# Performance work log

Measured on AMD Instinct MI355X. Metric: run time of the kernel, lower is better.

## Reference

```python
import jax, jax.numpy as jnp
import numpy as np

N, T, E, F, H, L, NC = 50000, 5, 500000, 64, 4, 2, 8192
NEG_SLOPE = 0.2  # PyG GATConv LeakyReLU slope


def _gat(x, src, dst, W, a_s, a_d, b):
    # x: [N,Fin], W: [Fin,H*F] -> h: [N,H,F]
    h = (x @ W).reshape(N, H, F)
    al = (h * a_s).sum(-1)                      # [N,H] alpha_src per node
    ar = (h * a_d).sum(-1)                      # [N,H] alpha_dst per node
    e = jax.nn.leaky_relu(al[src] + ar[dst], NEG_SLOPE)   # [Etot,H]
    m = jax.ops.segment_max(e, dst, num_segments=N)       # stable softmax per dst
    ex = jnp.exp(e - m[dst])
    den = jax.ops.segment_sum(ex, dst, num_segments=N)
    alpha = ex / (den[dst] + 1e-16)
    out = jax.ops.segment_sum(h[src] * alpha[:, :, None], dst, num_segments=N)
    return out.reshape(N, H * F) + b


def _gnn_stack(x, src, dst, gW, gas, gad, gb, lW, lb):
    for i in range(L):
        x = _gat(x, src, dst, gW[i], gas[i], gad[i], gb[i])
        x = jax.nn.relu(x @ lW[i] + lb[i])
    return x


def _snapshots(embeddings, edges, gW, gas, gad, gb, lW, lb):
    loop = jnp.arange(N)
    outs = []
    for t in range(T):
        src = jnp.concatenate([edges[t, 0], loop])  # add self loops (PyG default)
        dst = jnp.concatenate([edges[t, 1], loop])
        outs.append(_gnn_stack(embeddings[t], src, dst, gW, gas, gad, gb, lW, lb))
    # torch code prepends each snapshot -> time axis is reversed
    return jnp.stack(outs[::-1], axis=1)  # [N, T, F]


def _lstm(xs, Wi, Wh, b):
    # xs: [T,B,D]; torch gate order i,f,g,o
    B = xs.shape[1]
    hid = Wh.shape[1]
    def step(carry, x):
        h, c = carry
        g = x @ Wi.T + h @ Wh.T + b
        i, f, gg, o = jnp.split(g, 4, axis=-1)
        c = jax.nn.sigmoid(f) * c + jax.nn.sigmoid(i) * jnp.tanh(gg)
        h = jax.nn.sigmoid(o) * jnp.tanh(c)
        return (h, c), h
    init = (jnp.zeros((B, hid), xs.dtype), jnp.zeros((B, hid), xs.dtype))
    (hT, _), hs = jax.lax.scan(step, init, xs)
    return hs, hT


def setup_inputs() -> dict:
    key = jax.random.key(0)
    ks = iter(jax.random.split(key, 40))
    def nrm(shape, scale=0.1):
        return jax.random.normal(next(ks), shape, dtype=jnp.float32) * scale
    inp = {
        "embeddings": jax.random.normal(next(ks), (T, N, F), dtype=jnp.float32),
        "gat1_W": nrm((L, F, H * F)), "gat1_as": nrm((L, H, F)), "gat1_ad": nrm((L, H, F)), "gat1_b": nrm((L, H * F)),
        "lin1_W": nrm((L, H * F, F)), "lin1_b": nrm((L, F)),
        "gat2_W": nrm((L, F, H * F)), "gat2_as": nrm((L, H, F)), "gat2_ad": nrm((L, H, F)), "gat2_b": nrm((L, H * F)),
        "lin2_W": nrm((L, H * F, F)), "lin2_b": nrm((L, F)),
        "lstm1_Wi": nrm((4 * F, 2 * F)), "lstm1_Wh": nrm((4 * F, F)), "lstm1_b": nrm((4 * F,)),
        "lstm2_Wi": nrm((4 * F, F)), "lstm2_Wh": nrm((4 * F, F)), "lstm2_b": nrm((4 * F,)),
        "fc1_W": nrm((2 * F, F)), "fc1_b": nrm((F,)),
        "fc2_W": nrm((F, 2)), "fc2_b": nrm((2,)),
        "edges": jax.random.randint(next(ks), (T, 2, E), 0, N),
        "node_type": jax.random.randint(next(ks), (N,), 0, 4),
        "edge_type": jax.random.randint(next(ks), (T, E), 0, 4),
        "clf_neighbors": jax.random.randint(next(ks), (NC,), 0, N),
        "clf_nodes": jax.random.randint(next(ks), (NC,), 0, N),
    }
    return inp


def reference(embeddings, gat1_W, gat1_as, gat1_ad, gat1_b, lin1_W, lin1_b,
              gat2_W, gat2_as, gat2_ad, gat2_b, lin2_W, lin2_b,
              lstm1_Wi, lstm1_Wh, lstm1_b, lstm2_Wi, lstm2_Wh, lstm2_b,
              fc1_W, fc1_b, fc2_W, fc2_b,
              edges, node_type, edge_type, clf_neighbors, clf_nodes):
    e1 = _snapshots(embeddings, edges, gat1_W, gat1_as, gat1_ad, gat1_b, lin1_W, lin1_b)[clf_nodes]  # [NC,T,F]
    e2 = _snapshots(embeddings, edges, gat2_W, gat2_as, gat2_ad, gat2_b, lin2_W, lin2_b)[clf_nodes]
    seq = jnp.concatenate([e1, e2], axis=2).transpose(1, 0, 2)  # [T,NC,2F]; all lengths == T (clamp max=5)
    hs, h1 = _lstm(seq, lstm1_Wi, lstm1_Wh, lstm1_b)
    _, h2 = _lstm(hs, lstm2_Wi, lstm2_Wh, lstm2_b)
    z = jnp.concatenate([h1, h2], axis=1)        # [NC,2F]
    z = jax.nn.relu(z @ fc1_W + fc1_b)
    return jax.nn.relu(z @ fc2_W + fc2_b)        # [NC,2]
```

## Files before the change

kernel.cpp:

```cpp
#include <hip/hip_runtime.h>

#define NN 50000
#define TT 5
#define EE 500000
#define NC 8192
#define ET (EE + NN)
#define NCH 196

typedef unsigned short u16;
typedef __attribute__((ext_vector_type(8))) short bf16x8;
typedef __attribute__((ext_vector_type(4))) float f32x4;

__device__ __forceinline__ float lrelu(float x) { return x >= 0.f ? x : 0.2f * x; }
__device__ __forceinline__ float sigm(float x) { return 1.f / (1.f + expf(-x)); }
__device__ __forceinline__ float bf2f(u16 u) {
    union { unsigned int i; float f; } v; v.i = ((unsigned int)u) << 16; return v.f;
}
__device__ __forceinline__ u16 f2bf(float f) {
    unsigned int x = __float_as_uint(f);
    return (u16)((x + 0x7fffu + ((x >> 16) & 1u)) >> 16);
}
__device__ __forceinline__ ushort4 f4tobf(float4 v) {
    ushort4 u; u.x = f2bf(v.x); u.y = f2bf(v.y); u.z = f2bf(v.z); u.w = f2bf(v.w);
    return u;
}
__device__ __forceinline__ float4 bf4tof(ushort4 u) {
    return make_float4(bf2f(u.x), bf2f(u.y), bf2f(u.z), bf2f(u.w));
}

__global__ void k_fill1(int* p, int n) {
    int i = blockIdx.x * 256 + threadIdx.x;
    if (i < n) p[i] = 1;
}

__global__ void k_count(const int* __restrict__ edges, int* __restrict__ cnt) {
    int i = blockIdx.x * 256 + threadIdx.x;
    if (i >= TT * EE) return;
    int t = i / EE, e = i % EE;
    int dst = edges[(size_t)t * 2 * EE + EE + e];
    atomicAdd(&cnt[t * NN + dst], 1);
}

__global__ __launch_bounds__(256) void k_scan1(const int* __restrict__ cnt,
                                               int* __restrict__ sums) {
    int t = blockIdx.x / NCH, ch = blockIdx.x % NCH;
    int i = ch * 256 + threadIdx.x;
    int v = (i < NN) ? cnt[t * NN + i] : 0;
    __shared__ int s[256];
    s[threadIdx.x] = v;
    __syncthreads();
    for (int o = 128; o > 0; o >>= 1) {
        if (threadIdx.x < o) s[threadIdx.x] += s[threadIdx.x + o];
        __syncthreads();
    }
    if (threadIdx.x == 0) sums[t * NCH + ch] = s[0];
}

__global__ __launch_bounds__(256) void k_scan2(const int* __restrict__ sums,
                                               int* __restrict__ bases,
                                               int* __restrict__ off) {
    int t = blockIdx.x;
    __shared__ int s[256];
    int v = (threadIdx.x < NCH) ? sums[t * NCH + threadIdx.x] : 0;
    s[threadIdx.x] = v;
    __syncthreads();
    for (int o = 1; o < 256; o <<= 1) {
        int tv = (threadIdx.x >= o) ? s[threadIdx.x - o] : 0;
        __syncthreads();
        s[threadIdx.x] += tv;
        __syncthreads();
    }
    if (threadIdx.x < NCH) bases[t * NCH + threadIdx.x] = s[threadIdx.x] - v;
    if (threadIdx.x == 255) off[t * (NN + 1) + NN] = s[255];
}

__global__ __launch_bounds__(256) void k_scan3(int* __restrict__ cnt,
                                               const int* __restrict__ bases,
                                               int* __restrict__ off) {
    int t = blockIdx.x / NCH, ch = blockIdx.x % NCH;
    int i = ch * 256 + threadIdx.x;
    int v = (i < NN) ? cnt[t * NN + i] : 0;
    __shared__ int s[256];
    s[threadIdx.x] = v;
    __syncthreads();
    for (int o = 1; o < 256; o <<= 1) {
        int tv = (threadIdx.x >= o) ? s[threadIdx.x - o] : 0;
        __syncthreads();
        s[threadIdx.x] += tv;
        __syncthreads();
    }
    if (i < NN) {
        int excl = bases[t * NCH + ch] + s[threadIdx.x] - v;
        off[t * (NN + 1) + i] = excl;
        cnt[t * NN + i] = excl;
    }
}

__global__ void k_csrfill(const int* __restrict__ edges, int* __restrict__ fil,
                          int* __restrict__ csr) {
    int i = blockIdx.x * 256 + threadIdx.x;
    if (i >= TT * ET) return;
    int t = i / ET, r = i % ET;
    int src, dst;
    if (r < EE) {
        src = edges[(size_t)t * 2 * EE + r];
        dst = edges[(size_t)t * 2 * EE + EE + r];
    } else {
        src = dst = r - EE;
    }
    int pos = atomicAdd(&fil[t * NN + dst], 1);
    csr[(size_t)t * ET + pos] = src;
}

__global__ void k_transpose(const float* __restrict__ src, float* __restrict__ dst,
                            int R, int C) {
    int i = blockIdx.x * 256 + threadIdx.x;
    if (i >= R * C) return;
    int r = i / C, c = i % C;
    dst[c * R + r] = src[i];
}

__global__ void k_prep_wi1(const float* __restrict__ W, u16* __restrict__ Wb) {
    int i = blockIdx.x * 256 + threadIdx.x;
    if (i >= 256 * 128) return;
    Wb[i] = f2bf(W[i]);
}

__global__ void k_prep_was(const float* __restrict__ W,
                           const float* __restrict__ as_,
                           const float* __restrict__ ad_,
                           float* __restrict__ was, float* __restrict__ wad) {
    int id = blockIdx.x * 256 + threadIdx.x;
    if (id >= 2 * 64 * 4) return;
    int l = id >> 8, rem = id & 255;
    int k = rem >> 2, hd = rem & 3;
    float s = 0.f, d = 0.f;
    for (int f = 0; f < 64; ++f) {
        float w = W[(size_t)l * 16384 + k * 256 + hd * 64 + f];
        s += w * as_[l * 256 + hd * 64 + f];
        d += w * ad_[l * 256 + hd * 64 + f];
    }
    was[l * 256 + k * 4 + hd] = s;
    wad[l * 256 + k * 4 + hd] = d;
}

__global__ void k_prep_cmb(const float* __restrict__ W, const float* __restrict__ lW,
                           u16* __restrict__ CT) {
    int i = blockIdx.x * 256 + threadIdx.x;
    if (i >= 2 * 64 * 256) return;
    int l = i >> 14, rem = i & 16383;
    int f = rem >> 8, kk = rem & 255;
    int hd = kk >> 6, k = kk & 63;
    float s = 0.f;
    for (int j = 0; j < 64; ++j)
        s += W[(size_t)l * 16384 + k * 256 + hd * 64 + j] *
             lW[(size_t)l * 16384 + (hd * 64 + j) * 64 + f];
    CT[(size_t)l * 16384 + f * 256 + kk] = f2bf(s);
}

__global__ void k_prep_cb(const float* __restrict__ gb, const float* __restrict__ lW,
                          const float* __restrict__ lb, float* __restrict__ cb) {
    int i = blockIdx.x * 256 + threadIdx.x;
    if (i >= 2 * 64) return;
    int l = i >> 6, f = i & 63;
    float s = lb[l * 64 + f];
    for (int j = 0; j < 256; ++j)
        s += gb[l * 256 + j] * lW[(size_t)l * 16384 + j * 64 + f];
    cb[l * 64 + f] = s;
}

__global__ void k_f2bf4(const float* __restrict__ src, u16* __restrict__ dst, int n4) {
    int i = blockIdx.x * 256 + threadIdx.x;
    if (i >= n4) return;
    float4 f = ((const float4*)src)[i];
    ((ushort4*)dst)[i] = f4tobf(f);
}

__global__ void k_gather(const u16* __restrict__ x, const int* __restrict__ clf,
                         u16* __restrict__ dst) {
    int i = blockIdx.x * 256 + threadIdx.x;
    if (i >= NC * 16) return;
    int row = i >> 4, c4 = i & 15;
    int node = clf[row];
    ushort4 u = ((const ushort4*)x)[(size_t)node * 16 + c4];
    *(ushort4*)&dst[(size_t)row * 128 + c4 * 4] = u;
}

__global__ __launch_bounds__(256) void k_alar_x(const u16* __restrict__ xb,
                                                const float* __restrict__ was,
                                                const float* __restrict__ wad,
                                                float* __restrict__ al,
                                                float* __restrict__ ar) {
    int lane = threadIdx.x & 63;
    int n = blockIdx.x * 16 + (threadIdx.x >> 6) * 4 + (lane >> 4);
    int q = lane & 15;
    ushort4 u = *(const ushort4*)&xb[(size_t)n * 64 + q * 4];
    float ps[4] = {0.f, 0.f, 0.f, 0.f};
    float pd[4] = {0.f, 0.f, 0.f, 0.f};
#pragma unroll
    for (int d = 0; d < 4; ++d) {
        u16 uv = (d == 0) ? u.x : (d == 1) ? u.y : (d == 2) ? u.z : u.w;
        float xv = bf2f(uv);
        int k = q * 4 + d;
        float4 w4 = *(const float4*)&was[k * 4];
        float4 d4 = *(const float4*)&wad[k * 4];
        ps[0] += xv * w4.x; ps[1] += xv * w4.y;
        ps[2] += xv * w4.z; ps[3] += xv * w4.w;
        pd[0] += xv * d4.x; pd[1] += xv * d4.y;
        pd[2] += xv * d4.z; pd[3] += xv * d4.w;
    }
#pragma unroll
    for (int o = 1; o < 16; o <<= 1) {
#pragma unroll
        for (int hd = 0; hd < 4; ++hd) {
            ps[hd] += __shfl_xor(ps[hd], o, 64);
            pd[hd] += __shfl_xor(pd[hd], o, 64);
        }
    }
    if (q == 0) {
        *(float4*)&al[n * 4] = make_float4(ps[0], ps[1], ps[2], ps[3]);
        *(float4*)&ar[n * 4] = make_float4(pd[0], pd[1], pd[2], pd[3]);
    }
}

__global__ __launch_bounds__(256) void k_agg_x(const int* __restrict__ off,
                                               const int* __restrict__ csr,
                                               const float* __restrict__ al,
                                               const float* __restrict__ ar,
                                               const u16* __restrict__ xb,
                                               u16* __restrict__ xagg) {
    int lane = threadIdx.x & 63;
    int n = blockIdx.x * 4 + (threadIdx.x >> 6);
    int hh = lane & 3;
    int hf = lane >> 5;
    int kd = lane & 31;
    float ar_hh = ar[n * 4 + hh];
    int beg = off[n], end = off[n + 1];
    float den[4]  = {0.f, 0.f, 0.f, 0.f};
    float accL[4] = {0.f, 0.f, 0.f, 0.f};
    float accH[4] = {0.f, 0.f, 0.f, 0.f};

    for (int cbase = beg; cbase < end; cbase += 64) {
        int cnt = min(64, end - cbase);
        int sidx = csr[cbase + ((lane < cnt) ? lane : 0)];
        int nbat = (cnt + 15) >> 4;
        float pb[4];
#pragma unroll
        for (int b = 0; b < 4; ++b) {
            if (b < nbat) {
                int jj = b * 16 + (lane >> 2);
                int sj = __shfl(sidx, (jj < cnt) ? jj : 0, 64);
                pb[b] = expf(lrelu(al[sj * 4 + hh] + ar_hh));
            } else {
                pb[b] = 0.f;
            }
        }
        int R = (cnt + 1) >> 1;

#define LDX(r, dstv)                                                         \
        {                                                                    \
            int jj_ = (r) * 2 + hf;                                          \
            int ss_ = __shfl(sidx, (jj_ < cnt) ? jj_ : 0, 64);               \
            dstv = *(const unsigned*)&xb[(size_t)ss_ * 64 + kd * 2];         \
        }
#define CONS(r, cv)                                                          \
        {                                                                    \
            int je_ = (r) * 2 + hf;                                          \
            int b_ = ((r) >> 3) & 3;                                         \
            float pbb_ = (b_ == 0) ? pb[0] : (b_ == 1) ? pb[1]               \
                        : (b_ == 2) ? pb[2] : pb[3];                         \
            float xlo_ = bf2f((u16)((cv) & 0xffffu));                        \
            float xhi_ = bf2f((u16)((cv) >> 16));                            \
            _Pragma("unroll")                                                \
            for (int hd_ = 0; hd_ < 4; ++hd_) {                              \
                float p_ = __shfl(pbb_, ((je_ & 15) << 2) | hd_, 64);        \
                p_ = (je_ < cnt) ? p_ : 0.f;                                 \
                accL[hd_] += p_ * xlo_;                                      \
                accH[hd_] += p_ * xhi_;                                      \
                den[hd_]  += p_;                                             \
            }                                                                \
        }

        unsigned c0, c1, c2, c3;
        LDX(0, c0); LDX(1, c1); LDX(2, c2); LDX(3, c3);
        for (int g = 0; g < R; g += 4) {
            unsigned n0 = 0, n1 = 0, n2 = 0, n3 = 0;
            if (g + 4 < R) {
                LDX(g + 4, n0); LDX(g + 5, n1); LDX(g + 6, n2); LDX(g + 7, n3);
            }
            CONS(g + 0, c0);
            if (g + 1 < R) CONS(g + 1, c1);
            if (g + 2 < R) CONS(g + 2, c2);
            if (g + 3 < R) CONS(g + 3, c3);
            c0 = n0; c1 = n1; c2 = n2; c3 = n3;
        }
#undef LDX
#undef CONS
    }
#pragma unroll
    for (int hd = 0; hd < 4; ++hd) {
        accL[hd] += __shfl_xor(accL[hd], 32, 64);
        accH[hd] += __shfl_xor(accH[hd], 32, 64);
        den[hd]  += __shfl_xor(den[hd], 32, 64);
    }
    if (hf == 0) {
#pragma unroll
        for (int hd = 0; hd < 4; ++hd) {
            float inv = 1.f / (den[hd] + 1e-16f);
            unsigned w = (unsigned)f2bf(accL[hd] * inv) |
                         ((unsigned)f2bf(accH[hd] * inv) << 16);
            *(unsigned*)&xagg[(size_t)n * 256 + hd * 64 + kd * 2] = w;
        }
    }
}

__global__ __launch_bounds__(256) void k_gemm_cmb(const u16* __restrict__ A,
                                                  const u16* __restrict__ CT,
                                                  const float* __restrict__ cb,
                                                  u16* __restrict__ out,
                                                  const float* __restrict__ was2,
                                                  const float* __restrict__ wad2,
                                                  float* __restrict__ al1,
                                                  float* __restrict__ ar1) {
    int lane = threadIdx.x & 63;
    int wid = threadIdx.x >> 6;
    int g = lane >> 4, c = lane & 15;
    int r0 = blockIdx.x * 64 + wid * 16;
    int arow = r0 + c; if (arow > NN - 1) arow = NN - 1;
    const u16* aptr = A + (size_t)arow * 256 + g * 8;
    const u16* bptr = CT + (size_t)c * 256 + g * 8;
    f32x4 acc[4];
#pragma unroll
    for (int t = 0; t < 4; ++t) acc[t] = (f32x4){0.f, 0.f, 0.f, 0.f};
#pragma unroll
    for (int ks = 0; ks < 8; ++ks) {
        bf16x8 af = *(const bf16x8*)(aptr + ks * 32);
#pragma unroll
        for (int t = 0; t < 4; ++t) {
            bf16x8 bfr = *(const bf16x8*)(bptr + t * 16 * 256 + ks * 32);
            acc[t] = __builtin_amdgcn_mfma_f32_16x16x32_bf16(af, bfr, acc[t], 0, 0, 0);
        }
    }
    int orow0 = r0 + g * 4;
    float ps[4][4], pd[4][4];
#pragma unroll
    for (int j = 0; j < 4; ++j)
#pragma unroll
        for (int hd = 0; hd < 4; ++hd) { ps[j][hd] = 0.f; pd[j][hd] = 0.f; }
#pragma unroll
    for (int t = 0; t < 4; ++t) {
        int col = t * 16 + c;
        float bv = cb[col];
        float4 w4 = make_float4(0.f, 0.f, 0.f, 0.f), d4 = w4;
        if (al1) {
            w4 = *(const float4*)&was2[col * 4];
            d4 = *(const float4*)&wad2[col * 4];
        }
#pragma unroll
        for (int j = 0; j < 4; ++j) {
            int row = orow0 + j;
            float o = fmaxf(acc[t][j] + bv, 0.f);
            if (row < NN) out[(size_t)row * 64 + col] = f2bf(o);
            if (al1) {
                ps[j][0] += o * w4.x; ps[j][1] += o * w4.y;
                ps[j][2] += o * w4.z; ps[j][3] += o * w4.w;
                pd[j][0] += o * d4.x; pd[j][1] += o * d4.y;
                pd[j][2] += o * d4.z; pd[j][3] += o * d4.w;
            }
        }
    }
    if (al1) {
#pragma unroll
        for (int o = 1; o < 16; o <<= 1) {
#pragma unroll
            for (int j = 0; j < 4; ++j) {
#pragma unroll
                for (int hd = 0; hd < 4; ++hd) {
                    ps[j][hd] += __shfl_xor(ps[j][hd], o, 64);
                    pd[j][hd] += __shfl_xor(pd[j][hd], o, 64);
                }
            }
        }
        if (c == 0) {
#pragma unroll
            for (int j = 0; j < 4; ++j) {
                int row = orow0 + j;
                if (row < NN) {
                    *(float4*)&al1[row * 4] = make_float4(ps[j][0], ps[j][1], ps[j][2], ps[j][3]);
                    *(float4*)&ar1[row * 4] = make_float4(pd[j][0], pd[j][1], pd[j][2], pd[j][3]);
                }
            }
        }
    }
}

__global__ __launch_bounds__(256) void k_gemm_gx(const u16* __restrict__ A,
                                                 const u16* __restrict__ BT,
                                                 float* __restrict__ gxout, int M) {
    int lane = threadIdx.x & 63;
    int wid = threadIdx.x >> 6;
    int g = lane >> 4, c = lane & 15;
    int r0 = blockIdx.x * 64 + wid * 16;
    int arow = r0 + c; if (arow > M - 1) arow = M - 1;
    const u16* aptr = A + (size_t)arow * 128 + g * 8;
    f32x4 acc[16];
#pragma unroll
    for (int t = 0; t < 16; ++t) acc[t] = (f32x4){0.f, 0.f, 0.f, 0.f};
#pragma unroll
    for (int ks = 0; ks < 4; ++ks) {
        bf16x8 af = *(const bf16x8*)(aptr + ks * 32);
#pragma unroll
        for (int t = 0; t < 16; ++t) {
            bf16x8 bfr = *(const bf16x8*)(BT + (size_t)(t * 16 + c) * 128 + ks * 32 + g * 8);
            acc[t] = __builtin_amdgcn_mfma_f32_16x16x32_bf16(af, bfr, acc[t], 0, 0, 0);
        }
    }
#pragma unroll
    for (int t = 0; t < 16; ++t) {
#pragma unroll
        for (int j = 0; j < 4; ++j) {
            int row = r0 + g * 4 + j;
            if (row < M) gxout[(size_t)row * 256 + t * 16 + c] = acc[t][j];
        }
    }
}

__global__ __launch_bounds__(256) void k_lstm_fc(const float* __restrict__ gx,
                                                 const float* __restrict__ WhT1,
                                                 const float* __restrict__ bb1,
                                                 const float* __restrict__ WiT2,
                                                 const float* __restrict__ WhT2,
                                                 const float* __restrict__ bb2,
                                                 const float* __restrict__ fw1,
                                                 const float* __restrict__ fb1,
                                                 const float* __restrict__ fw2,
                                                 const float* __restrict__ fb2,
                                                 float* __restrict__ out) {
    __shared__ float xs[4][4][128];
    int w = threadIdx.x >> 6, lane = threadIdx.x & 63;
    int row0 = blockIdx.x * 16 + w * 4;
    float h1[4], c1[4], h2[4], c2[4];
#pragma unroll
    for (int r = 0; r < 4; ++r) { h1[r] = 0.f; c1[r] = 0.f; h2[r] = 0.f; c2[r] = 0.f; }
    float bi1 = bb1[lane], bf1 = bb1[64 + lane], bg1 = bb1[128 + lane], bo1 = bb1[192 + lane];
    float bi2 = bb2[lane], bf2v = bb2[64 + lane], bg2 = bb2[128 + lane], bo2 = bb2[192 + lane];

    for (int st = 0; st < TT; ++st) {
        int tsn = TT - 1 - st;
#pragma unroll
        for (int r = 0; r < 4; ++r) xs[w][r][lane] = h1[r];
        __syncthreads();
        {
            const float* gxp = gx + (size_t)tsn * NC * 256;
            float ai[4], af[4], ag[4], ao[4];
#pragma unroll
            for (int r = 0; r < 4; ++r) {
                const float* gr = gxp + (size_t)(row0 + r) * 256;
                ai[r] = bi1 + gr[lane];
                af[r] = bf1 + gr[64 + lane];
                ag[r] = bg1 + gr[128 + lane];
                ao[r] = bo1 + gr[192 + lane];
            }
            for (int k = 0; k < 64; ++k) {
                const float* wr = &WhT1[k * 256];
                float wi = wr[lane], wf = wr[64 + lane], wg = wr[128 + lane], wo = wr[192 + lane];
#pragma unroll
                for (int r = 0; r < 4; ++r) {
                    float hv = xs[w][r][k];
                    ai[r] += hv * wi; af[r] += hv * wf;
                    ag[r] += hv * wg; ao[r] += hv * wo;
                }
            }
#pragma unroll
            for (int r = 0; r < 4; ++r) {
                c1[r] = sigm(af[r]) * c1[r] + sigm(ai[r]) * tanhf(ag[r]);
                h1[r] = sigm(ao[r]) * tanhf(c1[r]);
            }
        }
        __syncthreads();
#pragma unroll
        for (int r = 0; r < 4; ++r) {
            xs[w][r][lane]      = h1[r];
            xs[w][r][64 + lane] = h2[r];
        }
        __syncthreads();
        {
            float ai[4], af[4], ag[4], ao[4];
#pragma unroll
            for (int r = 0; r < 4; ++r) { ai[r] = bi2; af[r] = bf2v; ag[r] = bg2; ao[r] = bo2; }
            for (int k = 0; k < 64; ++k) {
                const float* wr = &WiT2[k * 256];
                float wi = wr[lane], wf = wr[64 + lane], wg = wr[128 + lane], wo = wr[192 + lane];
#pragma unroll
                for (int r = 0; r < 4; ++r) {
                    float xv = xs[w][r][k];
                    ai[r] += xv * wi; af[r] += xv * wf;
                    ag[r] += xv * wg; ao[r] += xv * wo;
                }
            }
            for (int k = 0; k < 64; ++k) {
                const float* wr = &WhT2[k * 256];
                float wi = wr[lane], wf = wr[64 + lane], wg = wr[128 + lane], wo = wr[192 + lane];
#pragma unroll
                for (int r = 0; r < 4; ++r) {
                    float hv = xs[w][r][64 + k];
                    ai[r] += hv * wi; af[r] += hv * wf;
                    ag[r] += hv * wg; ao[r] += hv * wo;
                }
            }
#pragma unroll
            for (int r = 0; r < 4; ++r) {
                c2[r] = sigm(af[r]) * c2[r] + sigm(ai[r]) * tanhf(ag[r]);
                h2[r] = sigm(ao[r]) * tanhf(c2[r]);
            }
        }
        __syncthreads();
    }
#pragma unroll
    for (int r = 0; r < 4; ++r) {
        xs[w][r][lane]      = h1[r];
        xs[w][r][64 + lane] = h2[r];
    }
    __syncthreads();
    float acc[4];
#pragma unroll
    for (int r = 0; r < 4; ++r) acc[r] = fb1[lane];
    for (int k = 0; k < 128; ++k) {
        float wv = fw1[k * 64 + lane];
#pragma unroll
        for (int r = 0; r < 4; ++r) acc[r] += xs[w][r][k] * wv;
    }
    float w20 = fw2[lane * 2], w21 = fw2[lane * 2 + 1];
#pragma unroll
    for (int r = 0; r < 4; ++r) {
        float rr = fmaxf(acc[r], 0.f);
        float t0 = rr * w20;
        float t1 = rr * w21;
#pragma unroll
        for (int o = 32; o >= 1; o >>= 1) {
            t0 += __shfl_xor(t0, o, 64);
            t1 += __shfl_xor(t1, o, 64);
        }
        if (lane == 0) {
            out[(row0 + r) * 2]     = fmaxf(t0 + fb2[0], 0.f);
            out[(row0 + r) * 2 + 1] = fmaxf(t1 + fb2[1], 0.f);
        }
    }
}

extern "C" void kernel_launch(void* const* d_in, const int* in_sizes, int n_in,
                              void* d_out, int out_size, void* d_ws, size_t ws_size,
                              hipStream_t stream) {
    const float* emb  = (const float*)d_in[0];
    const float* g1W  = (const float*)d_in[1];
    const float* g1as = (const float*)d_in[2];
    const float* g1ad = (const float*)d_in[3];
    const float* g1b  = (const float*)d_in[4];
    const float* l1W  = (const float*)d_in[5];
    const float* l1b  = (const float*)d_in[6];
    const float* g2W  = (const float*)d_in[7];
    const float* g2as = (const float*)d_in[8];
    const float* g2ad = (const float*)d_in[9];
    const float* g2b  = (const float*)d_in[10];
    const float* l2W  = (const float*)d_in[11];
    const float* l2b  = (const float*)d_in[12];
    const float* Wi1  = (const float*)d_in[13];
    const float* Wh1  = (const float*)d_in[14];
    const float* b1   = (const float*)d_in[15];
    const float* Wi2  = (const float*)d_in[16];
    const float* Wh2  = (const float*)d_in[17];
    const float* b2   = (const float*)d_in[18];
    const float* fc1W = (const float*)d_in[19];
    const float* fc1b = (const float*)d_in[20];
    const float* fc2W = (const float*)d_in[21];
    const float* fc2b = (const float*)d_in[22];
    const int* edges = (const int*)d_in[23];
    const int* clf   = (const int*)d_in[27];

    char* ws = (char*)d_ws;
    size_t woff = 0;
    auto alloc = [&](size_t bytes) -> void* {
        void* p = ws + woff;
        woff += (bytes + 255) & ~(size_t)255;
        return p;
    };
    int* csr_off  = (int*)alloc((size_t)TT * (NN + 1) * 4);
    int* csr_fil  = (int*)alloc((size_t)TT * NN * 4);
    int* csr_src  = (int*)alloc((size_t)TT * ET * 4);
    int* scan_sum = (int*)alloc((size_t)TT * NCH * 4);
    int* scan_bas = (int*)alloc((size_t)TT * NCH * 4);
    u16* embb     = (u16*)alloc((size_t)TT * NN * 64 * 2);
    u16* xbuf     = (u16*)alloc((size_t)NN * 64 * 2);
    u16* xaggb    = (u16*)alloc((size_t)NN * 256 * 2);
    float* al0    = (float*)alloc((size_t)TT * NN * 4 * 4);
    float* ar0    = (float*)alloc((size_t)TT * NN * 4 * 4);
    float* al1    = (float*)alloc((size_t)NN * 4 * 4);
    float* ar1    = (float*)alloc((size_t)NN * 4 * 4);
    u16* seq2     = (u16*)alloc((size_t)TT * NC * 128 * 2);
    float* gxb    = (float*)alloc((size_t)TT * NC * 256 * 4);
    float* WhT1   = (float*)alloc(64 * 256 * 4);
    float* WiT2   = (float*)alloc(64 * 256 * 4);
    float* WhT2   = (float*)alloc(64 * 256 * 4);
    u16* wi1b     = (u16*)alloc((size_t)256 * 128 * 2);
    u16* CT1      = (u16*)alloc((size_t)2 * 64 * 256 * 2);
    u16* CT2      = (u16*)alloc((size_t)2 * 64 * 256 * 2);
    float* cb1    = (float*)alloc((size_t)2 * 64 * 4);
    float* cb2    = (float*)alloc((size_t)2 * 64 * 4);
    float* wasb1  = (float*)alloc((size_t)2 * 64 * 4 * 4);
    float* wadb1  = (float*)alloc((size_t)2 * 64 * 4 * 4);
    float* wasb2  = (float*)alloc((size_t)2 * 64 * 4 * 4);
    float* wadb2  = (float*)alloc((size_t)2 * 64 * 4 * 4);

    k_fill1<<<(TT * NN + 255) / 256, 256, 0, stream>>>(csr_fil, TT * NN);
    k_count<<<(TT * EE + 255) / 256, 256, 0, stream>>>(edges, csr_fil);
    k_scan1<<<TT * NCH, 256, 0, stream>>>(csr_fil, scan_sum);
    k_scan2<<<TT, 256, 0, stream>>>(scan_sum, scan_bas, csr_off);
    k_scan3<<<TT * NCH, 256, 0, stream>>>(csr_fil, scan_bas, csr_off);
    k_csrfill<<<(TT * ET + 255) / 256, 256, 0, stream>>>(edges, csr_fil, csr_src);

    k_transpose<<<(256 * 64 + 255) / 256, 256, 0, stream>>>(Wh1, WhT1, 256, 64);
    k_transpose<<<(256 * 64 + 255) / 256, 256, 0, stream>>>(Wi2, WiT2, 256, 64);
    k_transpose<<<(256 * 64 + 255) / 256, 256, 0, stream>>>(Wh2, WhT2, 256, 64);
    k_prep_wi1<<<(256 * 128 + 255) / 256, 256, 0, stream>>>(Wi1, wi1b);
    k_prep_was<<<2, 256, 0, stream>>>(g1W, g1as, g1ad, wasb1, wadb1);
    k_prep_was<<<2, 256, 0, stream>>>(g2W, g2as, g2ad, wasb2, wadb2);
    k_prep_cmb<<<(2 * 64 * 256 + 255) / 256, 256, 0, stream>>>(g1W, l1W, CT1);
    k_prep_cmb<<<(2 * 64 * 256 + 255) / 256, 256, 0, stream>>>(g2W, l2W, CT2);
    k_prep_cb<<<1, 256, 0, stream>>>(g1b, l1W, l1b, cb1);
    k_prep_cb<<<1, 256, 0, stream>>>(g2b, l2W, l2b, cb2);
    k_f2bf4<<<(TT * NN * 16 + 255) / 256, 256, 0, stream>>>(emb, embb, TT * NN * 16);

    for (int s = 0; s < 2; ++s) {
        const float* was = s ? wasb2 : wasb1;
        const float* wad = s ? wadb2 : wadb1;
        const u16* CT    = s ? CT2 : CT1;
        const float* cbp = s ? cb2 : cb1;
        k_alar_x<<<(TT * NN) / 16, 256, 0, stream>>>(
            embb, was + 0 * 256, wad + 0 * 256, al0, ar0);
        for (int t = 0; t < TT; ++t) {
            k_agg_x<<<NN / 4, 256, 0, stream>>>(
                csr_off + (size_t)t * (NN + 1), csr_src + (size_t)t * ET,
                al0 + (size_t)t * NN * 4, ar0 + (size_t)t * NN * 4,
                embb + (size_t)t * NN * 64, xaggb);
            k_gemm_cmb<<<(NN + 63) / 64, 256, 0, stream>>>(
                xaggb, CT + (size_t)0 * 16384, cbp + 0 * 64, xbuf,
                was + 1 * 256, wad + 1 * 256, al1, ar1);
            k_agg_x<<<NN / 4, 256, 0, stream>>>(
                csr_off + (size_t)t * (NN + 1), csr_src + (size_t)t * ET,
                al1, ar1, xbuf, xaggb);
            k_gemm_cmb<<<(NN + 63) / 64, 256, 0, stream>>>(
                xaggb, CT + (size_t)1 * 16384, cbp + 1 * 64, xbuf,
                nullptr, nullptr, nullptr, nullptr);
            k_gather<<<(NC * 16 + 255) / 256, 256, 0, stream>>>(
                xbuf, clf, seq2 + (size_t)t * NC * 128 + s * 64);
        }
    }

    k_gemm_gx<<<(TT * NC + 63) / 64, 256, 0, stream>>>(seq2, wi1b, gxb, TT * NC);

    k_lstm_fc<<<NC / 16, 256, 0, stream>>>(
        gxb, WhT1, b1, WiT2, WhT2, b2,
        fc1W, fc1b, fc2W, fc2b, (float*)d_out);
}
```

Before: 1.695 ms.

## Batch all snapshots into single aggregation, GEMM and gather launches

The per-snapshot loop that issued five kernels per snapshot is replaced by one launch per stage that covers all five snapshots. Each kernel derives its snapshot index from the block or thread index and offsets into per-snapshot CSR, attention and feature buffers. The intermediate buffers are enlarged to hold all snapshots, and the LSTM gate buffer now reuses the aggregation buffer's memory. This removes launch gaps and small-grid tail effects, at the cost of a much larger working set (about 128 MB for the aggregation buffer) that may fit the on-chip caches less well.

Result: faster. 1.459 ms (-13.9%).

```diff
diff --git a/kernel.cpp b/kernel.cpp
--- a/kernel.cpp
+++ b/kernel.cpp
@@ -179,11 +179,12 @@
 __global__ void k_gather(const u16* __restrict__ x, const int* __restrict__ clf,
                          u16* __restrict__ dst) {
     int i = blockIdx.x * 256 + threadIdx.x;
-    if (i >= NC * 16) return;
-    int row = i >> 4, c4 = i & 15;
+    if (i >= TT * NC * 16) return;
+    int t = i / (NC * 16), rem = i % (NC * 16);
+    int row = rem >> 4, c4 = rem & 15;
     int node = clf[row];
-    ushort4 u = ((const ushort4*)x)[(size_t)node * 16 + c4];
-    *(ushort4*)&dst[(size_t)row * 128 + c4 * 4] = u;
+    ushort4 u = ((const ushort4*)(x + (size_t)t * NN * 64))[(size_t)node * 16 + c4];
+    *(ushort4*)&dst[((size_t)t * NC + row) * 128 + c4 * 4] = u;
 }
 
 __global__ __launch_bounds__(256) void k_alar_x(const u16* __restrict__ xb,
@@ -229,20 +230,27 @@
                                                const float* __restrict__ ar,
                                                const u16* __restrict__ xb,
                                                u16* __restrict__ xagg) {
+    const int bpt = NN / 4;
     int lane = threadIdx.x & 63;
-    int n = blockIdx.x * 4 + (threadIdx.x >> 6);
+    int t = blockIdx.x / bpt;
+    int n = (blockIdx.x % bpt) * 4 + (threadIdx.x >> 6);
+    const int* offp = off + (size_t)t * (NN + 1);
+    const int* csrp = csr + (size_t)t * ET;
+    const float* alp = al + (size_t)t * NN * 4;
+    const u16* xbp = xb + (size_t)t * NN * 64;
+    u16* xap = xagg + (size_t)t * NN * 256;
     int hh = lane & 3;
     int hf = lane >> 5;
     int kd = lane & 31;
-    float ar_hh = ar[n * 4 + hh];
-    int beg = off[n], end = off[n + 1];
+    float ar_hh = ar[(size_t)t * NN * 4 + n * 4 + hh];
+    int beg = offp[n], end = offp[n + 1];
     float den[4]  = {0.f, 0.f, 0.f, 0.f};
     float accL[4] = {0.f, 0.f, 0.f, 0.f};
     float accH[4] = {0.f, 0.f, 0.f, 0.f};
 
     for (int cbase = beg; cbase < end; cbase += 64) {
         int cnt = min(64, end - cbase);
-        int sidx = csr[cbase + ((lane < cnt) ? lane : 0)];
+        int sidx = csrp[cbase + ((lane < cnt) ? lane : 0)];
         int nbat = (cnt + 15) >> 4;
         float pb[4];
 #pragma unroll
@@ -250,7 +258,7 @@
             if (b < nbat) {
                 int jj = b * 16 + (lane >> 2);
                 int sj = __shfl(sidx, (jj < cnt) ? jj : 0, 64);
-                pb[b] = expf(lrelu(al[sj * 4 + hh] + ar_hh));
+                pb[b] = expf(lrelu(alp[sj * 4 + hh] + ar_hh));
             } else {
                 pb[b] = 0.f;
             }
@@ -261,9 +269,9 @@
         {                                                                    \
             int jj_ = (r) * 2 + hf;                                          \
             int ss_ = __shfl(sidx, (jj_ < cnt) ? jj_ : 0, 64);               \
-            dstv = *(const unsigned*)&xb[(size_t)ss_ * 64 + kd * 2];         \
-        }
-#define CONS(r, cv)                                                          \
+            dstv = *(const unsigned*)&xbp[(size_t)ss_ * 64 + kd * 2];        \
+        }
+#define CONS(r, cv)                                                         \
         {                                                                    \
             int je_ = (r) * 2 + hf;                                          \
             int b_ = ((r) >> 3) & 3;                                         \
@@ -309,7 +317,7 @@
             float inv = 1.f / (den[hd] + 1e-16f);
             unsigned w = (unsigned)f2bf(accL[hd] * inv) |
                          ((unsigned)f2bf(accH[hd] * inv) << 16);
-            *(unsigned*)&xagg[(size_t)n * 256 + hd * 64 + kd * 2] = w;
+            *(unsigned*)&xap[(size_t)n * 256 + hd * 64 + kd * 2] = w;
         }
     }
 }
@@ -317,7 +325,7 @@
 __global__ __launch_bounds__(256) void k_gemm_cmb(const u16* __restrict__ A,
                                                   const u16* __restrict__ CT,
                                                   const float* __restrict__ cb,
-                                                  u16* __restrict__ out,
+                                                  u16* __restrict__ out, int M,
                                                   const float* __restrict__ was2,
                                                   const float* __restrict__ wad2,
                                                   float* __restrict__ al1,
@@ -326,7 +334,7 @@
     int wid = threadIdx.x >> 6;
     int g = lane >> 4, c = lane & 15;
     int r0 = blockIdx.x * 64 + wid * 16;
-    int arow = r0 + c; if (arow > NN - 1) arow = NN - 1;
+    int arow = r0 + c; if (arow > M - 1) arow = M - 1;
     const u16* aptr = A + (size_t)arow * 256 + g * 8;
     const u16* bptr = CT + (size_t)c * 256 + g * 8;
     f32x4 acc[4];
@@ -360,7 +368,7 @@
         for (int j = 0; j < 4; ++j) {
             int row = orow0 + j;
             float o = fmaxf(acc[t][j] + bv, 0.f);
-            if (row < NN) out[(size_t)row * 64 + col] = f2bf(o);
+            if (row < M) out[(size_t)row * 64 + col] = f2bf(o);
             if (al1) {
                 ps[j][0] += o * w4.x; ps[j][1] += o * w4.y;
                 ps[j][2] += o * w4.z; ps[j][3] += o * w4.w;
@@ -385,7 +393,7 @@
 #pragma unroll
             for (int j = 0; j < 4; ++j) {
                 int row = orow0 + j;
-                if (row < NN) {
+                if (row < M) {
                     *(float4*)&al1[row * 4] = make_float4(ps[j][0], ps[j][1], ps[j][2], ps[j][3]);
                     *(float4*)&ar1[row * 4] = make_float4(pd[j][0], pd[j][1], pd[j][2], pd[j][3]);
                 }
@@ -590,14 +598,14 @@
     int* scan_sum = (int*)alloc((size_t)TT * NCH * 4);
     int* scan_bas = (int*)alloc((size_t)TT * NCH * 4);
     u16* embb     = (u16*)alloc((size_t)TT * NN * 64 * 2);
-    u16* xbuf     = (u16*)alloc((size_t)NN * 64 * 2);
-    u16* xaggb    = (u16*)alloc((size_t)NN * 256 * 2);
+    u16* xbuf5    = (u16*)alloc((size_t)TT * NN * 64 * 2);
+    u16* xaggb    = (u16*)alloc((size_t)TT * NN * 256 * 2);
     float* al0    = (float*)alloc((size_t)TT * NN * 4 * 4);
     float* ar0    = (float*)alloc((size_t)TT * NN * 4 * 4);
-    float* al1    = (float*)alloc((size_t)NN * 4 * 4);
-    float* ar1    = (float*)alloc((size_t)NN * 4 * 4);
+    float* al1    = (float*)alloc((size_t)TT * NN * 4 * 4);
+    float* ar1    = (float*)alloc((size_t)TT * NN * 4 * 4);
     u16* seq2     = (u16*)alloc((size_t)TT * NC * 128 * 2);
-    float* gxb    = (float*)alloc((size_t)TT * NC * 256 * 4);
+    float* gxb    = (float*)xaggb;
     float* WhT1   = (float*)alloc(64 * 256 * 4);
     float* WiT2   = (float*)alloc(64 * 256 * 4);
     float* WhT2   = (float*)alloc(64 * 256 * 4);
@@ -630,30 +638,26 @@
     k_prep_cb<<<1, 256, 0, stream>>>(g2b, l2W, l2b, cb2);
     k_f2bf4<<<(TT * NN * 16 + 255) / 256, 256, 0, stream>>>(emb, embb, TT * NN * 16);
 
+    const int MB = TT * NN;
     for (int s = 0; s < 2; ++s) {
         const float* was = s ? wasb2 : wasb1;
         const float* wad = s ? wadb2 : wadb1;
         const u16* CT    = s ? CT2 : CT1;
         const float* cbp = s ? cb2 : cb1;
-        k_alar_x<<<(TT * NN) / 16, 256, 0, stream>>>(
+        k_alar_x<<<MB / 16, 256, 0, stream>>>(
             embb, was + 0 * 256, wad + 0 * 256, al0, ar0);
-        for (int t = 0; t < TT; ++t) {
-            k_agg_x<<<NN / 4, 256, 0, stream>>>(
-                csr_off + (size_t)t * (NN + 1), csr_src + (size_t)t * ET,
-                al0 + (size_t)t * NN * 4, ar0 + (size_t)t * NN * 4,
-                embb + (size_t)t * NN * 64, xaggb);
-            k_gemm_cmb<<<(NN + 63) / 64, 256, 0, stream>>>(
-                xaggb, CT + (size_t)0 * 16384, cbp + 0 * 64, xbuf,
-                was + 1 * 256, wad + 1 * 256, al1, ar1);
-            k_agg_x<<<NN / 4, 256, 0, stream>>>(
-                csr_off + (size_t)t * (NN + 1), csr_src + (size_t)t * ET,
-                al1, ar1, xbuf, xaggb);
-            k_gemm_cmb<<<(NN + 63) / 64, 256, 0, stream>>>(
-                xaggb, CT + (size_t)1 * 16384, cbp + 1 * 64, xbuf,
-                nullptr, nullptr, nullptr, nullptr);
-            k_gather<<<(NC * 16 + 255) / 256, 256, 0, stream>>>(
-                xbuf, clf, seq2 + (size_t)t * NC * 128 + s * 64);
-        }
+        k_agg_x<<<TT * (NN / 4), 256, 0, stream>>>(
+            csr_off, csr_src, al0, ar0, embb, xaggb);
+        k_gemm_cmb<<<(MB + 63) / 64, 256, 0, stream>>>(
+            xaggb, CT + (size_t)0 * 16384, cbp + 0 * 64, xbuf5, MB,
+            was + 1 * 256, wad + 1 * 256, al1, ar1);
+        k_agg_x<<<TT * (NN / 4), 256, 0, stream>>>(
+            csr_off, csr_src, al1, ar1, xbuf5, xaggb);
+        k_gemm_cmb<<<(MB + 63) / 64, 256, 0, stream>>>(
+            xaggb, CT + (size_t)1 * 16384, cbp + 1 * 64, xbuf5, MB,
+            nullptr, nullptr, nullptr, nullptr);
+        k_gather<<<(TT * NC * 16 + 255) / 256, 256, 0, stream>>>(
+            xbuf5, clf, seq2 + s * 64);
     }
 
     k_gemm_gx<<<(TT * NC + 63) / 64, 256, 0, stream>>>(seq2, wi1b, gxb, TT * NC);
```
